# Performance work log

Measured on AMD Instinct MI355X. Metric: run time of the kernel, lower is better.

Reference implementation:

```python
import jax, jax.numpy as jnp
import numpy as np

EMBED_DIM = 1024
N_HEADS = 16
HEAD_DIM = EMBED_DIM // N_HEADS
N_TOKENS = 65536


def setup_inputs() -> dict:
    key = jax.random.key(0)
    ks = jax.random.split(key, 5)
    scale = 1.0 / np.sqrt(EMBED_DIM)
    return {
        "x": jax.random.normal(ks[0], (N_TOKENS, EMBED_DIM), dtype=jnp.float32),
        "Wq": jax.random.normal(ks[1], (EMBED_DIM, EMBED_DIM), dtype=jnp.float32) * scale,
        "Wk": jax.random.normal(ks[2], (EMBED_DIM, EMBED_DIM), dtype=jnp.float32) * scale,
        "Wv": jax.random.normal(ks[3], (EMBED_DIM, EMBED_DIM), dtype=jnp.float32) * scale,
        "Wo": jax.random.normal(ks[4], (EMBED_DIM, EMBED_DIM), dtype=jnp.float32) * scale,
    }


def reference(x, Wq, Wk, Wv, Wo):
    # Linear layers (torch nn.Linear: y = x @ W^T, bias=False)
    q = x @ Wq.T  # [N, E]
    k = x @ Wk.T
    v = x @ Wv.T
    n = x.shape[0]
    q = q.reshape(n, N_HEADS, HEAD_DIM)  # [N, H, D]
    k = k.reshape(n, N_HEADS, HEAD_DIM)
    v = v.reshape(n, N_HEADS, HEAD_DIM)
    # Faithful to original: attention across the HEAD axis per token -> [N, H, H]
    scores = jnp.einsum("nhd,ngd->nhg", q, k) / jnp.sqrt(jnp.asarray(HEAD_DIM, x.dtype))
    attn = jax.nn.softmax(scores, axis=-1)  # [N, H, H]
    out = jnp.einsum("nhg,ngd->nhd", attn, v).reshape(n, EMBED_DIM)
    return out @ Wo.T
```

## Files before the change

### kernel.cpp

```cpp
#include <hip/hip_runtime.h>
#include <hip/hip_bf16.h>
#include <cstdint>

#define DEV static __device__ __forceinline__

typedef __attribute__((ext_vector_type(8))) __bf16 bf16x8;
typedef __attribute__((ext_vector_type(4))) float f32x4;
typedef __attribute__((ext_vector_type(8))) unsigned short ushort8;

constexpr int NTOK = 65536;
constexpr int E = 1024;

DEV unsigned short f2b(float f) {
  unsigned int u = __builtin_bit_cast(unsigned int, f);
  u += 0x7fffu + ((u >> 16) & 1u);
  return (unsigned short)(u >> 16);
}

DEV f32x4 mfma16(bf16x8 a, bf16x8 b, f32x4 c) {
  return __builtin_amdgcn_mfma_f32_16x16x32_bf16(a, b, c, 0, 0, 0);
}

DEV void gload16(const void* g, const void* l) {
  __builtin_amdgcn_global_load_lds(
      (const __attribute__((address_space(1))) void*)g,
      (__attribute__((address_space(3))) void*)l, 16, 0, 0);
}

DEV void BAR() {
  asm volatile("" ::: "memory");
  __builtin_amdgcn_s_barrier();
  asm volatile("" ::: "memory");
  __builtin_amdgcn_sched_barrier(0);
}

#define WAITVM(n_) do { \
  asm volatile("s_waitcnt vmcnt(" #n_ ")" ::: "memory"); \
  __builtin_amdgcn_sched_barrier(0); \
} while (0)

#define WAITLGKM0() do { \
  asm volatile("s_waitcnt lgkmcnt(0)" ::: "memory"); \
  __builtin_amdgcn_sched_barrier(0); \
} while (0)

__global__ void cvt8(const float* __restrict__ in, unsigned short* __restrict__ out,
                     int n8) {
  int i = blockIdx.x * blockDim.x + threadIdx.x;
  if (i >= n8) return;
  const float4* p = (const float4*)(in + (size_t)i * 8);
  float4 a = p[0], b = p[1];
  ushort8 r;
  r[0] = f2b(a.x); r[1] = f2b(a.y); r[2] = f2b(a.z); r[3] = f2b(a.w);
  r[4] = f2b(b.x); r[5] = f2b(b.y); r[6] = f2b(b.z); r[7] = f2b(b.w);
  *(ushort8*)(out + (size_t)i * 8) = r;
}

template <typename OutT>
__global__ __launch_bounds__(512, 2) void gemm8(
    const unsigned short* __restrict__ A, const unsigned short* __restrict__ B,
    OutT* __restrict__ C, int M, int N, int K, int nbx) {
  __shared__ char smem[131072];
  char* sA = smem;
  char* sB = smem + 65536;

  const int NT = K >> 6;
  const int nwg = gridDim.x;
  const int cpx = nwg >> 3;
  const int wg = ((int)blockIdx.x & 7) * cpx + ((int)blockIdx.x >> 3);
  const int tm = (wg / nbx) * 256;
  const int tn = (wg % nbx) * 256;

  const int t = threadIdx.x;
  const int w = t >> 6, l = t & 63;
  const int wr = w >> 2, wc = w & 3;
  const int lr = l & 15, q = l >> 4;

  const int srow = w * 8 + (l >> 3);
  const int scol = ((l & 7) ^ (l >> 3)) * 8;
  const int xorv = (lr & 7) << 4;
  const int offk0 = (q * 16) ^ xorv;
  const int offk1 = (64 + q * 16) ^ xorv;
  const int aRB = wr * 8192 + lr * 128;
  const int bRB = wc * 4096 + lr * 128;

#define STAGE_A(tt_, h_) do { \
    const unsigned short* g_ = A + (size_t)(tm + (h_)*128 + srow) * K + (tt_)*64 + scol; \
    const char* d_ = sA + (((tt_) & 1) * 32768 + (h_)*16384 + w * 1024); \
    gload16(g_, d_); \
    gload16(g_ + (size_t)64 * K, d_ + 8192); \
  } while (0)

#define STAGE_B(tt_, h_) do { \
    const unsigned short* g_ = B + (size_t)(tn + (h_)*128 + srow) * K + (tt_)*64 + scol; \
    const char* d_ = sB + (((tt_) & 1) * 32768 + (h_)*16384 + w * 1024); \
    gload16(g_, d_); \
    gload16(g_ + (size_t)64 * K, d_ + 8192); \
  } while (0)

  f32x4 acc[8][4] = {};
  bf16x8 af[4][2];
  bf16x8 bf_[2][2][2];

#define LDA(buf_, mh_) do { \
    _Pragma("unroll") for (int m_ = 0; m_ < 4; ++m_) { \
      af[m_][0] = *(const bf16x8*)(sA + (buf_)*32768 + (mh_)*16384 + m_*2048 + aRB + offk0); \
      af[m_][1] = *(const bf16x8*)(sA + (buf_)*32768 + (mh_)*16384 + m_*2048 + aRB + offk1); \
    } \
  } while (0)

#define LDB(buf_, nh_) do { \
    _Pragma("unroll") for (int n_ = 0; n_ < 2; ++n_) { \
      bf_[nh_][n_][0] = *(const bf16x8*)(sB + (buf_)*32768 + (nh_)*16384 + n_*2048 + bRB + offk0); \
      bf_[nh_][n_][1] = *(const bf16x8*)(sB + (buf_)*32768 + (nh_)*16384 + n_*2048 + bRB + offk1); \
    } \
  } while (0)

#define MM(mh_, nh_) do { \
    __builtin_amdgcn_s_setprio(1); \
    _Pragma("unroll") for (int m_ = 0; m_ < 4; ++m_) \
      _Pragma("unroll") for (int n_ = 0; n_ < 2; ++n_) { \
        acc[(mh_)*4 + m_][(nh_)*2 + n_] = \
            mfma16(af[m_][0], bf_[nh_][n_][0], acc[(mh_)*4 + m_][(nh_)*2 + n_]); \
        acc[(mh_)*4 + m_][(nh_)*2 + n_] = \
            mfma16(af[m_][1], bf_[nh_][n_][1], acc[(mh_)*4 + m_][(nh_)*2 + n_]); \
      } \
    __builtin_amdgcn_s_setprio(0); \
  } while (0)

  STAGE_A(0, 0); STAGE_B(0, 0); STAGE_B(0, 1); STAGE_A(0, 1);
  STAGE_A(1, 0); STAGE_B(1, 0); STAGE_B(1, 1);
  WAITVM(6);
  BAR();

  int T = 0;
  for (; T + 3 < NT; T += 2) {
    LDA(0, 0); LDB(0, 0);
    STAGE_A(T + 1, 1);
    BAR(); MM(0, 0); BAR();
    LDB(0, 1);
    STAGE_A(T + 2, 0);
    BAR(); MM(0, 1); BAR();
    LDA(0, 1);
    STAGE_B(T + 2, 0);
    BAR(); MM(1, 0); BAR();
    STAGE_B(T + 2, 1);
    WAITVM(6);
    BAR(); MM(1, 1); BAR();
    LDA(1, 0); LDB(1, 0);
    STAGE_A(T + 2, 1);
    BAR(); MM(0, 0); BAR();
    LDB(1, 1);
    STAGE_A(T + 3, 0);
    BAR(); MM(0, 1); BAR();
    LDA(1, 1);
    STAGE_B(T + 3, 0);
    BAR(); MM(1, 0); BAR();
    STAGE_B(T + 3, 1);
    WAITVM(6);
    BAR(); MM(1, 1); BAR();
  }
  {
    LDA(0, 0); LDB(0, 0);
    STAGE_A(T + 1, 1);
    BAR(); MM(0, 0); BAR();
    LDB(0, 1);
    BAR(); MM(0, 1); BAR();
    LDA(0, 1);
    BAR(); MM(1, 0); BAR();
    WAITVM(0);
    BAR(); MM(1, 1); BAR();
    LDA(1, 0); LDB(1, 0);
    BAR(); MM(0, 0); BAR();
    LDB(1, 1);
    BAR(); MM(0, 1); BAR();
    LDA(1, 1);
    BAR(); MM(1, 0); BAR();
    BAR(); MM(1, 1); BAR();
  }

#pragma unroll
  for (int mh = 0; mh < 2; ++mh)
#pragma unroll
    for (int m = 0; m < 4; ++m)
#pragma unroll
      for (int nh = 0; nh < 2; ++nh)
#pragma unroll
        for (int n = 0; n < 2; ++n)
#pragma unroll
          for (int j = 0; j < 4; ++j) {
            int row = tm + mh * 128 + wr * 64 + m * 16 + q * 4 + j;
            int col = tn + nh * 128 + wc * 32 + n * 16 + lr;
            float v = acc[mh * 4 + m][nh * 2 + n][j];
            if constexpr (sizeof(OutT) == 2)
              C[(size_t)row * N + col] = (OutT)f2b(v);
            else
              C[(size_t)row * N + col] = v;
          }
#undef STAGE_A
#undef STAGE_B
#undef LDA
#undef LDB
#undef MM
}

__global__ __launch_bounds__(256, 4) void attn16(
    const unsigned short* __restrict__ qkv, unsigned short* __restrict__ out) {
  __shared__ unsigned short P[4][16 * 16];
  const int t = threadIdx.x, w = t >> 6, l = t & 63;
  const int tok = blockIdx.x * 4 + w;
  const unsigned short* q = qkv + (size_t)tok * 3072;
  const unsigned short* kp = q + 1024;
  const unsigned short* vp = q + 2048;
  const int lr = l & 15, lk = (l >> 4) * 8;
  bf16x8 aq0 = *reinterpret_cast<const bf16x8*>(q + lr * 64 + lk);
  bf16x8 aq1 = *reinterpret_cast<const bf16x8*>(q + lr * 64 + 32 + lk);
  bf16x8 bk0 = *reinterpret_cast<const bf16x8*>(kp + lr * 64 + lk);
  bf16x8 bk1 = *reinterpret_cast<const bf16x8*>(kp + lr * 64 + 32 + lk);
  f32x4 s = {};
  s = mfma16(aq0, bk0, s);
  s = mfma16(aq1, bk1, s);
  const float cexp = 0.125f * 1.44269504f;
  float p[4];
#pragma unroll
  for (int j = 0; j < 4; ++j) {
    float m = s[j];
    m = fmaxf(m, __shfl_xor(m, 1));
    m = fmaxf(m, __shfl_xor(m, 2));
    m = fmaxf(m, __shfl_xor(m, 4));
    m = fmaxf(m, __shfl_xor(m, 8));
    float e = exp2f((s[j] - m) * cexp);
    float sum = e;
    sum += __shfl_xor(sum, 1);
    sum += __shfl_xor(sum, 2);
    sum += __shfl_xor(sum, 4);
    sum += __shfl_xor(sum, 8);
    p[j] = e / sum;
  }
  unsigned short* Pw = P[w];
#pragma unroll
  for (int j = 0; j < 4; ++j) Pw[((l >> 4) * 4 + j) * 16 + lr] = f2b(p[j]);
  WAITLGKM0();
  ushort8 zz = {0, 0, 0, 0, 0, 0, 0, 0};
  bf16x8 ap = __builtin_bit_cast(bf16x8, zz);
  bf16x8 bv[4];
#pragma unroll
  for (int b = 0; b < 4; ++b) bv[b] = ap;
  if (l < 32) {
    ap = *reinterpret_cast<const bf16x8*>(&Pw[lr * 16 + lk]);
#pragma unroll
    for (int b = 0; b < 4; ++b) {
      ushort8 tmp;
#pragma unroll
      for (int j = 0; j < 8; ++j) tmp[j] = vp[(lk + j) * 64 + b * 16 + lr];
      bv[b] = __builtin_bit_cast(bf16x8, tmp);
    }
  }
  f32x4 o[4] = {};
#pragma unroll
  for (int b = 0; b < 4; ++b) o[b] = mfma16(ap, bv[b], o[b]);
  unsigned short* op = out + (size_t)tok * 1024;
#pragma unroll
  for (int b = 0; b < 4; ++b)
#pragma unroll
    for (int j = 0; j < 4; ++j)
      op[((l >> 4) * 4 + j) * 64 + b * 16 + lr] = f2b(o[b][j]);
}

extern "C" void kernel_launch(void* const* d_in, const int* in_sizes, int n_in,
                              void* d_out, int out_size, void* d_ws, size_t ws_size,
                              hipStream_t stream) {
  const float* x = (const float*)d_in[0];
  const float* Wq = (const float*)d_in[1];
  const float* Wk = (const float*)d_in[2];
  const float* Wv = (const float*)d_in[3];
  const float* Wo = (const float*)d_in[4];

  unsigned short* xb = (unsigned short*)d_ws;
  unsigned short* wqkv = xb + (size_t)NTOK * E;
  unsigned short* wo = wqkv + (size_t)3 * E * E;
  unsigned short* qkv = wo + (size_t)E * E;
  unsigned short* att = qkv + (size_t)NTOK * 3 * E;

  cvt8<<<(NTOK * E / 8) / 256, 256, 0, stream>>>(x, xb, NTOK * E / 8);
  cvt8<<<(E * E / 8) / 256, 256, 0, stream>>>(Wq, wqkv, E * E / 8);
  cvt8<<<(E * E / 8) / 256, 256, 0, stream>>>(Wk, wqkv + E * E, E * E / 8);
  cvt8<<<(E * E / 8) / 256, 256, 0, stream>>>(Wv, wqkv + 2 * E * E, E * E / 8);
  cvt8<<<(E * E / 8) / 256, 256, 0, stream>>>(Wo, wo, E * E / 8);

  gemm8<unsigned short><<<(NTOK / 256) * (3 * E / 256), 512, 0, stream>>>(
      xb, wqkv, qkv, NTOK, 3 * E, E, 3 * E / 256);

  attn16<<<NTOK / 4, 256, 0, stream>>>(qkv, att);

  gemm8<float><<<(NTOK / 256) * (E / 256), 512, 0, stream>>>(
      att, wo, (float*)d_out, NTOK, E, E, E / 256);
}
```

Baseline: 747.6 us.

## Make GEMMs persistent with cross-tile prefetch and fuse weight conversions

Replaces the one-tile-per-workgroup GEMM with a persistent kernel launched on 256 workgroups. Each workgroup loops over several output tiles and prefetches the next tile's first K slices while finishing the current one, hiding prologue and epilogue latency. K is hardcoded to 1024, with shift-based addressing. The four weight conversion launches are merged into one kernel to cut launch overhead. The trade-off is that the store epilogue is serialized inside the persistent loop and the kernel no longer handles general K.

Measured after the change: 1.278 ms. 1.71x slower.

```diff
diff --git a/kernel.cpp b/kernel.cpp
--- a/kernel.cpp
+++ b/kernel.cpp
@@ -56,20 +56,31 @@
   *(ushort8*)(out + (size_t)i * 8) = r;
 }
 
+__global__ void cvtW(const float* __restrict__ Wq, const float* __restrict__ Wk,
+                     const float* __restrict__ Wv, const float* __restrict__ Wo,
+                     unsigned short* __restrict__ out) {
+  int i = blockIdx.x * blockDim.x + threadIdx.x;
+  int wsel = i >> 17;
+  const float* src = wsel == 0 ? Wq : wsel == 1 ? Wk : wsel == 2 ? Wv : Wo;
+  int j = i & 131071;
+  const float4* p = (const float4*)(src + (size_t)j * 8);
+  float4 a = p[0], b = p[1];
+  ushort8 r;
+  r[0] = f2b(a.x); r[1] = f2b(a.y); r[2] = f2b(a.z); r[3] = f2b(a.w);
+  r[4] = f2b(b.x); r[5] = f2b(b.y); r[6] = f2b(b.z); r[7] = f2b(b.w);
+  *(ushort8*)(out + (size_t)i * 8) = r;
+}
+
 template <typename OutT>
-__global__ __launch_bounds__(512, 2) void gemm8(
+__global__ __launch_bounds__(512, 2) void gemmp(
     const unsigned short* __restrict__ A, const unsigned short* __restrict__ B,
-    OutT* __restrict__ C, int M, int N, int K, int nbx) {
+    OutT* __restrict__ C, int N, int nbx, int rounds) {
   __shared__ char smem[131072];
   char* sA = smem;
   char* sB = smem + 65536;
 
-  const int NT = K >> 6;
-  const int nwg = gridDim.x;
-  const int cpx = nwg >> 3;
-  const int wg = ((int)blockIdx.x & 7) * cpx + ((int)blockIdx.x >> 3);
-  const int tm = (wg / nbx) * 256;
-  const int tn = (wg % nbx) * 256;
+  const int tiles = rounds << 8;
+  const int cpx = tiles >> 3;
 
   const int t = threadIdx.x;
   const int w = t >> 6, l = t & 63;
@@ -78,24 +89,33 @@
 
   const int srow = w * 8 + (l >> 3);
   const int scol = ((l & 7) ^ (l >> 3)) * 8;
+  const size_t voff = (size_t)srow * 1024 + scol;
   const int xorv = (lr & 7) << 4;
   const int offk0 = (q * 16) ^ xorv;
   const int offk1 = (64 + q * 16) ^ xorv;
   const int aRB = wr * 8192 + lr * 128;
   const int bRB = wc * 4096 + lr * 128;
 
-#define STAGE_A(tt_, h_) do { \
-    const unsigned short* g_ = A + (size_t)(tm + (h_)*128 + srow) * K + (tt_)*64 + scol; \
-    const char* d_ = sA + (((tt_) & 1) * 32768 + (h_)*16384 + w * 1024); \
+  int tm, tn;
+  {
+    int v = (int)blockIdx.x;
+    int wg = (v & 7) * cpx + (v >> 3);
+    tm = (wg / nbx) << 8;
+    tn = (wg % nbx) << 8;
+  }
+
+#define STAGE_A(base_, kk_, h_) do { \
+    const unsigned short* g_ = A + (((size_t)((base_) + (h_)*128)) << 10) + ((kk_) << 6) + voff; \
+    const char* d_ = sA + ((((kk_) & 1) << 15) + (h_)*16384 + w * 1024); \
     gload16(g_, d_); \
-    gload16(g_ + (size_t)64 * K, d_ + 8192); \
-  } while (0)
-
-#define STAGE_B(tt_, h_) do { \
-    const unsigned short* g_ = B + (size_t)(tn + (h_)*128 + srow) * K + (tt_)*64 + scol; \
-    const char* d_ = sB + (((tt_) & 1) * 32768 + (h_)*16384 + w * 1024); \
+    gload16(g_ + (size_t)(64 << 10), d_ + 8192); \
+  } while (0)
+
+#define STAGE_B(base_, kk_, h_) do { \
+    const unsigned short* g_ = B + (((size_t)((base_) + (h_)*128)) << 10) + ((kk_) << 6) + voff; \
+    const char* d_ = sB + ((((kk_) & 1) << 15) + (h_)*16384 + w * 1024); \
     gload16(g_, d_); \
-    gload16(g_ + (size_t)64 * K, d_ + 8192); \
+    gload16(g_ + (size_t)(64 << 10), d_ + 8192); \
   } while (0)
 
   f32x4 acc[8][4] = {};
@@ -128,75 +148,116 @@
     __builtin_amdgcn_s_setprio(0); \
   } while (0)
 
-  STAGE_A(0, 0); STAGE_B(0, 0); STAGE_B(0, 1); STAGE_A(0, 1);
-  STAGE_A(1, 0); STAGE_B(1, 0); STAGE_B(1, 1);
+  STAGE_A(tm, 0, 0); STAGE_B(tn, 0, 0); STAGE_B(tn, 0, 1); STAGE_A(tm, 0, 1);
+  STAGE_A(tm, 1, 0); STAGE_B(tn, 1, 0); STAGE_B(tn, 1, 1);
   WAITVM(6);
   BAR();
 
-  int T = 0;
-  for (; T + 3 < NT; T += 2) {
-    LDA(0, 0); LDB(0, 0);
-    STAGE_A(T + 1, 1);
-    BAR(); MM(0, 0); BAR();
-    LDB(0, 1);
-    STAGE_A(T + 2, 0);
-    BAR(); MM(0, 1); BAR();
-    LDA(0, 1);
-    STAGE_B(T + 2, 0);
-    BAR(); MM(1, 0); BAR();
-    STAGE_B(T + 2, 1);
-    WAITVM(6);
-    BAR(); MM(1, 1); BAR();
-    LDA(1, 0); LDB(1, 0);
-    STAGE_A(T + 2, 1);
-    BAR(); MM(0, 0); BAR();
-    LDB(1, 1);
-    STAGE_A(T + 3, 0);
-    BAR(); MM(0, 1); BAR();
-    LDA(1, 1);
-    STAGE_B(T + 3, 0);
-    BAR(); MM(1, 0); BAR();
-    STAGE_B(T + 3, 1);
-    WAITVM(6);
-    BAR(); MM(1, 1); BAR();
+#pragma unroll 1
+  for (int r = 0; r < rounds; ++r) {
+    const bool last = (r == rounds - 1);
+    int tmn = tm, tnn = tn;
+    if (!last) {
+      int v = (int)blockIdx.x + (r + 1) * 256;
+      int wg = (v & 7) * cpx + (v >> 3);
+      tmn = (wg / nbx) << 8;
+      tnn = (wg % nbx) << 8;
+    }
+#pragma unroll 1
+    for (int T = 0; T < 14; T += 2) {
+      LDA(0, 0); LDB(0, 0);
+      STAGE_A(tm, T + 1, 1);
+      BAR(); MM(0, 0); BAR();
+      LDB(0, 1);
+      STAGE_A(tm, T + 2, 0);
+      BAR(); MM(0, 1); BAR();
+      LDA(0, 1);
+      STAGE_B(tn, T + 2, 0);
+      BAR(); MM(1, 0); BAR();
+      STAGE_B(tn, T + 2, 1);
+      WAITVM(6);
+      BAR(); MM(1, 1); BAR();
+      LDA(1, 0); LDB(1, 0);
+      STAGE_A(tm, T + 2, 1);
+      BAR(); MM(0, 0); BAR();
+      LDB(1, 1);
+      STAGE_A(tm, T + 3, 0);
+      BAR(); MM(0, 1); BAR();
+      LDA(1, 1);
+      STAGE_B(tn, T + 3, 0);
+      BAR(); MM(1, 0); BAR();
+      STAGE_B(tn, T + 3, 1);
+      WAITVM(6);
+      BAR(); MM(1, 1); BAR();
+    }
+    if (!last) {
+      LDA(0, 0); LDB(0, 0);
+      STAGE_A(tm, 15, 1);
+      BAR(); MM(0, 0); BAR();
+      LDB(0, 1);
+      STAGE_A(tmn, 0, 0);
+      BAR(); MM(0, 1); BAR();
+      LDA(0, 1);
+      STAGE_B(tnn, 0, 0);
+      BAR(); MM(1, 0); BAR();
+      STAGE_B(tnn, 0, 1);
+      WAITVM(6);
+      BAR(); MM(1, 1); BAR();
+      LDA(1, 0); LDB(1, 0);
+      STAGE_A(tmn, 0, 1);
+      BAR(); MM(0, 0); BAR();
+      LDB(1, 1);
+      STAGE_A(tmn, 1, 0);
+      BAR(); MM(0, 1); BAR();
+      LDA(1, 1);
+      STAGE_B(tnn, 1, 0);
+      BAR(); MM(1, 0); BAR();
+      STAGE_B(tnn, 1, 1);
+      WAITVM(6);
+      BAR(); MM(1, 1); BAR();
+    } else {
+      LDA(0, 0); LDB(0, 0);
+      STAGE_A(tm, 15, 1);
+      BAR(); MM(0, 0); BAR();
+      LDB(0, 1);
+      BAR(); MM(0, 1); BAR();
+      LDA(0, 1);
+      BAR(); MM(1, 0); BAR();
+      WAITVM(0);
+      BAR(); MM(1, 1); BAR();
+      LDA(1, 0); LDB(1, 0);
+      BAR(); MM(0, 0); BAR();
+      LDB(1, 1);
+      BAR(); MM(0, 1); BAR();
+      LDA(1, 1);
+      BAR(); MM(1, 0); BAR();
+      BAR(); MM(1, 1); BAR();
+    }
+#pragma unroll
+    for (int mh = 0; mh < 2; ++mh)
+#pragma unroll
+      for (int m = 0; m < 4; ++m)
+#pragma unroll
+        for (int nh = 0; nh < 2; ++nh)
+#pragma unroll
+          for (int n = 0; n < 2; ++n)
+#pragma unroll
+            for (int j = 0; j < 4; ++j) {
+              int row = tm + mh * 128 + wr * 64 + m * 16 + q * 4 + j;
+              int col = tn + nh * 128 + wc * 32 + n * 16 + lr;
+              float v = acc[mh * 4 + m][nh * 2 + n][j];
+              if constexpr (sizeof(OutT) == 2)
+                C[(size_t)row * N + col] = (OutT)f2b(v);
+              else
+                C[(size_t)row * N + col] = v;
+            }
+#pragma unroll
+    for (int i = 0; i < 8; ++i)
+#pragma unroll
+      for (int jj = 0; jj < 4; ++jj) acc[i][jj] = (f32x4){0.f, 0.f, 0.f, 0.f};
+    tm = tmn;
+    tn = tnn;
   }
-  {
-    LDA(0, 0); LDB(0, 0);
-    STAGE_A(T + 1, 1);
-    BAR(); MM(0, 0); BAR();
-    LDB(0, 1);
-    BAR(); MM(0, 1); BAR();
-    LDA(0, 1);
-    BAR(); MM(1, 0); BAR();
-    WAITVM(0);
-    BAR(); MM(1, 1); BAR();
-    LDA(1, 0); LDB(1, 0);
-    BAR(); MM(0, 0); BAR();
-    LDB(1, 1);
-    BAR(); MM(0, 1); BAR();
-    LDA(1, 1);
-    BAR(); MM(1, 0); BAR();
-    BAR(); MM(1, 1); BAR();
-  }
-
-#pragma unroll
-  for (int mh = 0; mh < 2; ++mh)
-#pragma unroll
-    for (int m = 0; m < 4; ++m)
-#pragma unroll
-      for (int nh = 0; nh < 2; ++nh)
-#pragma unroll
-        for (int n = 0; n < 2; ++n)
-#pragma unroll
-          for (int j = 0; j < 4; ++j) {
-            int row = tm + mh * 128 + wr * 64 + m * 16 + q * 4 + j;
-            int col = tn + nh * 128 + wc * 32 + n * 16 + lr;
-            float v = acc[mh * 4 + m][nh * 2 + n][j];
-            if constexpr (sizeof(OutT) == 2)
-              C[(size_t)row * N + col] = (OutT)f2b(v);
-            else
-              C[(size_t)row * N + col] = v;
-          }
 #undef STAGE_A
 #undef STAGE_B
 #undef LDA
@@ -283,16 +344,11 @@
   unsigned short* att = qkv + (size_t)NTOK * 3 * E;
 
   cvt8<<<(NTOK * E / 8) / 256, 256, 0, stream>>>(x, xb, NTOK * E / 8);
-  cvt8<<<(E * E / 8) / 256, 256, 0, stream>>>(Wq, wqkv, E * E / 8);
-  cvt8<<<(E * E / 8) / 256, 256, 0, stream>>>(Wk, wqkv + E * E, E * E / 8);
-  cvt8<<<(E * E / 8) / 256, 256, 0, stream>>>(Wv, wqkv + 2 * E * E, E * E / 8);
-  cvt8<<<(E * E / 8) / 256, 256, 0, stream>>>(Wo, wo, E * E / 8);
-
-  gemm8<unsigned short><<<(NTOK / 256) * (3 * E / 256), 512, 0, stream>>>(
-      xb, wqkv, qkv, NTOK, 3 * E, E, 3 * E / 256);
+  cvtW<<<(4 * E * E / 8) / 256, 256, 0, stream>>>(Wq, Wk, Wv, Wo, wqkv);
+
+  gemmp<unsigned short><<<256, 512, 0, stream>>>(xb, wqkv, qkv, 3 * E, 12, 12);
 
   attn16<<<NTOK / 4, 256, 0, stream>>>(qkv, att);
 
-  gemm8<float><<<(NTOK / 256) * (E / 256), 512, 0, stream>>>(
-      att, wo, (float*)d_out, NTOK, E, E, E / 256);
-}
+  gemmp<float><<<256, 512, 0, stream>>>(att, wo, (float*)d_out, E, 4, 4);
+}
```

## Switch GEMM to 32x32x16 MFMA tiles and merge weight conversions into one launch

Applied to the files above, without the earlier changes.

The GEMM inner product now uses 32x32x16 bf16 MFMA instructions instead of 16x16x32, with reorganised LDS fragment loads, accumulator layout and epilogue indexing to match. Larger MFMA tiles give more math per LDS fragment read and fewer instructions per tile. Separately, the four weight fp32-to-bf16 conversion launches are merged into one kernel to cut launch overhead. The wider accumulators change register use, and the new LDS read pattern may cause bank conflicts under the existing swizzle.

New measurement: 814.2 us. +8.9%, slower.

```diff
diff --git a/kernel.cpp b/kernel.cpp
--- a/kernel.cpp
+++ b/kernel.cpp
@@ -6,6 +6,7 @@
 
 typedef __attribute__((ext_vector_type(8))) __bf16 bf16x8;
 typedef __attribute__((ext_vector_type(4))) float f32x4;
+typedef __attribute__((ext_vector_type(16))) float f32x16;
 typedef __attribute__((ext_vector_type(8))) unsigned short ushort8;
 
 constexpr int NTOK = 65536;
@@ -19,6 +20,10 @@
 
 DEV f32x4 mfma16(bf16x8 a, bf16x8 b, f32x4 c) {
   return __builtin_amdgcn_mfma_f32_16x16x32_bf16(a, b, c, 0, 0, 0);
+}
+
+DEV f32x16 mfma32(bf16x8 a, bf16x8 b, f32x16 c) {
+  return __builtin_amdgcn_mfma_f32_32x32x16_bf16(a, b, c, 0, 0, 0);
 }
 
 DEV void gload16(const void* g, const void* l) {
@@ -56,6 +61,21 @@
   *(ushort8*)(out + (size_t)i * 8) = r;
 }
 
+__global__ void cvtW(const float* __restrict__ Wq, const float* __restrict__ Wk,
+                     const float* __restrict__ Wv, const float* __restrict__ Wo,
+                     unsigned short* __restrict__ out) {
+  int i = blockIdx.x * blockDim.x + threadIdx.x;
+  int wsel = i >> 17;
+  const float* src = wsel == 0 ? Wq : wsel == 1 ? Wk : wsel == 2 ? Wv : Wo;
+  int j = i & 131071;
+  const float4* p = (const float4*)(src + (size_t)j * 8);
+  float4 a = p[0], b = p[1];
+  ushort8 r;
+  r[0] = f2b(a.x); r[1] = f2b(a.y); r[2] = f2b(a.z); r[3] = f2b(a.w);
+  r[4] = f2b(b.x); r[5] = f2b(b.y); r[6] = f2b(b.z); r[7] = f2b(b.w);
+  *(ushort8*)(out + (size_t)i * 8) = r;
+}
+
 template <typename OutT>
 __global__ __launch_bounds__(512, 2) void gemm8(
     const unsigned short* __restrict__ A, const unsigned short* __restrict__ B,
@@ -74,15 +94,14 @@
   const int t = threadIdx.x;
   const int w = t >> 6, l = t & 63;
   const int wr = w >> 2, wc = w & 3;
-  const int lr = l & 15, q = l >> 4;
+  const int arL = l & 31;
+  const int kh = (l >> 5) * 16;
 
   const int srow = w * 8 + (l >> 3);
   const int scol = ((l & 7) ^ (l >> 3)) * 8;
-  const int xorv = (lr & 7) << 4;
-  const int offk0 = (q * 16) ^ xorv;
-  const int offk1 = (64 + q * 16) ^ xorv;
-  const int aRB = wr * 8192 + lr * 128;
-  const int bRB = wc * 4096 + lr * 128;
+  const int xorv = (l & 7) << 4;
+  const int aRB = wr * 8192 + arL * 128;
+  const int bRB = wc * 4096 + arL * 128;
 
 #define STAGE_A(tt_, h_) do { \
     const unsigned short* g_ = A + (size_t)(tm + (h_)*128 + srow) * K + (tt_)*64 + scol; \
@@ -98,33 +117,29 @@
     gload16(g_ + (size_t)64 * K, d_ + 8192); \
   } while (0)
 
-  f32x4 acc[8][4] = {};
-  bf16x8 af[4][2];
-  bf16x8 bf_[2][2][2];
+  f32x16 acc[4][2] = {};
+  bf16x8 af[2][4];
+  bf16x8 bB[2][4];
 
 #define LDA(buf_, mh_) do { \
-    _Pragma("unroll") for (int m_ = 0; m_ < 4; ++m_) { \
-      af[m_][0] = *(const bf16x8*)(sA + (buf_)*32768 + (mh_)*16384 + m_*2048 + aRB + offk0); \
-      af[m_][1] = *(const bf16x8*)(sA + (buf_)*32768 + (mh_)*16384 + m_*2048 + aRB + offk1); \
-    } \
+    _Pragma("unroll") for (int i_ = 0; i_ < 2; ++i_) \
+      _Pragma("unroll") for (int ks_ = 0; ks_ < 4; ++ks_) \
+        af[i_][ks_] = *(const bf16x8*)(sA + (buf_)*32768 + (mh_)*16384 + aRB + \
+                                       i_*4096 + ((ks_*32 + kh) ^ xorv)); \
   } while (0)
 
 #define LDB(buf_, nh_) do { \
-    _Pragma("unroll") for (int n_ = 0; n_ < 2; ++n_) { \
-      bf_[nh_][n_][0] = *(const bf16x8*)(sB + (buf_)*32768 + (nh_)*16384 + n_*2048 + bRB + offk0); \
-      bf_[nh_][n_][1] = *(const bf16x8*)(sB + (buf_)*32768 + (nh_)*16384 + n_*2048 + bRB + offk1); \
-    } \
+    _Pragma("unroll") for (int ks_ = 0; ks_ < 4; ++ks_) \
+      bB[nh_][ks_] = *(const bf16x8*)(sB + (buf_)*32768 + (nh_)*16384 + bRB + \
+                                      ((ks_*32 + kh) ^ xorv)); \
   } while (0)
 
 #define MM(mh_, nh_) do { \
     __builtin_amdgcn_s_setprio(1); \
-    _Pragma("unroll") for (int m_ = 0; m_ < 4; ++m_) \
-      _Pragma("unroll") for (int n_ = 0; n_ < 2; ++n_) { \
-        acc[(mh_)*4 + m_][(nh_)*2 + n_] = \
-            mfma16(af[m_][0], bf_[nh_][n_][0], acc[(mh_)*4 + m_][(nh_)*2 + n_]); \
-        acc[(mh_)*4 + m_][(nh_)*2 + n_] = \
-            mfma16(af[m_][1], bf_[nh_][n_][1], acc[(mh_)*4 + m_][(nh_)*2 + n_]); \
-      } \
+    _Pragma("unroll") for (int ks_ = 0; ks_ < 4; ++ks_) \
+      _Pragma("unroll") for (int i_ = 0; i_ < 2; ++i_) \
+        acc[(mh_)*2 + i_][nh_] = \
+            mfma32(af[i_][ks_], bB[nh_][ks_], acc[(mh_)*2 + i_][nh_]); \
     __builtin_amdgcn_s_setprio(0); \
   } while (0)
 
@@ -182,21 +197,19 @@
 #pragma unroll
   for (int mh = 0; mh < 2; ++mh)
 #pragma unroll
-    for (int m = 0; m < 4; ++m)
+    for (int i = 0; i < 2; ++i)
 #pragma unroll
       for (int nh = 0; nh < 2; ++nh)
 #pragma unroll
-        for (int n = 0; n < 2; ++n)
-#pragma unroll
-          for (int j = 0; j < 4; ++j) {
-            int row = tm + mh * 128 + wr * 64 + m * 16 + q * 4 + j;
-            int col = tn + nh * 128 + wc * 32 + n * 16 + lr;
-            float v = acc[mh * 4 + m][nh * 2 + n][j];
-            if constexpr (sizeof(OutT) == 2)
-              C[(size_t)row * N + col] = (OutT)f2b(v);
-            else
-              C[(size_t)row * N + col] = v;
-          }
+        for (int j = 0; j < 16; ++j) {
+          int row = tm + mh * 128 + wr * 64 + i * 32 + (l >> 5) * 4 + (j & 3) + 8 * (j >> 2);
+          int col = tn + nh * 128 + wc * 32 + arL;
+          float v = acc[mh * 2 + i][nh][j];
+          if constexpr (sizeof(OutT) == 2)
+            C[(size_t)row * N + col] = (OutT)f2b(v);
+          else
+            C[(size_t)row * N + col] = v;
+        }
 #undef STAGE_A
 #undef STAGE_B
 #undef LDA
@@ -283,10 +296,7 @@
   unsigned short* att = qkv + (size_t)NTOK * 3 * E;
 
   cvt8<<<(NTOK * E / 8) / 256, 256, 0, stream>>>(x, xb, NTOK * E / 8);
-  cvt8<<<(E * E / 8) / 256, 256, 0, stream>>>(Wq, wqkv, E * E / 8);
-  cvt8<<<(E * E / 8) / 256, 256, 0, stream>>>(Wk, wqkv + E * E, E * E / 8);
-  cvt8<<<(E * E / 8) / 256, 256, 0, stream>>>(Wv, wqkv + 2 * E * E, E * E / 8);
-  cvt8<<<(E * E / 8) / 256, 256, 0, stream>>>(Wo, wo, E * E / 8);
+  cvtW<<<(4 * E * E / 8) / 256, 256, 0, stream>>>(Wq, Wk, Wv, Wo, wqkv);
 
   gemm8<unsigned short><<<(NTOK / 256) * (3 * E / 256), 512, 0, stream>>>(
       xb, wqkv, qkv, NTOK, 3 * E, E, 3 * E / 256);
```
